# Kernel optimization log

Measured on AMD Instinct MI355X. Metric: run time of the kernel, lower is better.

The kernel has to match this reference:

```python
import jax, jax.numpy as jnp
import numpy as np

# (npoint, radius, nsample) per SA stage, from module defaults
SA_CFG = [(2048, 0.2, 64), (1024, 0.4, 32), (512, 0.6, 16), (256, 1.2, 8)]


def fps(xyz, npoint):
    """Farthest point sampling, CUDA-kernel semantics: start at index 0.
    xyz: [B,N,3] -> idx [B,npoint] int32."""
    B, N, _ = xyz.shape

    def step(carry, _):
        dist, far = carry
        centroid = jnp.take_along_axis(xyz, far[:, None, None], axis=1)  # [B,1,3]
        d = jnp.sum((xyz - centroid) ** 2, axis=-1)                      # [B,N]
        dist = jnp.minimum(dist, d)
        return (dist, jnp.argmax(dist, axis=-1).astype(jnp.int32)), far

    init = (jnp.full((B, N), 1e10, xyz.dtype), jnp.zeros((B,), jnp.int32))
    _, idxs = jax.lax.scan(step, init, None, length=npoint)  # [npoint,B]
    return idxs.T


def gather(pts, idx):
    """pts: [B,N,C], idx: [B,...] int -> [B,...,C]."""
    return jax.vmap(lambda p, i: p[i])(pts, idx)


def ball_query(xyz, new_xyz, radius, nsample):
    """First-nsample-in-ball semantics of pointnet2 ball_query; pads with the
    first found neighbor. xyz:[B,N,3], new_xyz:[B,S,3] -> [B,S,nsample] int."""
    N = xyz.shape[1]
    # squared dists via ||a||^2 + ||b||^2 - 2ab to avoid a [B,S,N,3] temp
    d2 = (jnp.sum(new_xyz ** 2, -1)[:, :, None]
          + jnp.sum(xyz ** 2, -1)[:, None, :]
          - 2.0 * jnp.einsum('bsc,bnc->bsn', new_xyz, xyz))
    cand = jnp.where(d2 < radius * radius, jnp.arange(N)[None, None, :], N)
    idx = jnp.sort(cand, axis=-1)[..., :nsample]
    first = idx[..., :1]  # center itself is always in the ball (d2==0)
    return jnp.where(idx == N, first, idx)


def sa_stage(xyz, feats, npoint, radius, nsample, layers):
    """One PointnetSAModuleVotes: FPS + ball query + normalized relative xyz
    (use_xyz=True, normalize_xyz=True) + shared MLP + max pool over nsample."""
    fidx = fps(xyz, npoint)
    new_xyz = gather(xyz, fidx)                         # [B,S,3]
    nidx = ball_query(xyz, new_xyz, radius, nsample)    # [B,S,K]
    rel = (gather(xyz, nidx) - new_xyz[:, :, None, :]) / radius  # [B,S,K,3]
    x = rel if feats is None else jnp.concatenate([rel, gather(feats, nidx)], -1)
    for w, b in layers:  # shared 1x1-conv MLP (BN folded), ReLU
        x = jax.nn.relu(x @ w + b)
    return new_xyz, jnp.max(x, axis=2)                  # [B,S,C_out]


def setup_inputs() -> dict:
    key = jax.random.key(0)
    ks = jax.random.split(key, 16)
    inp = {"pointcloud": jax.random.normal(ks[0], (4, 16384, 3), jnp.float32)}
    dims = [(3, 64, 64, 128), (131, 128, 128, 256),
            (259, 256, 256, 512), (515, 512, 512, 512)]
    k = 1
    for s, d in enumerate(dims, 1):
        for l in range(3):
            inp[f"w{s}{l}"] = jax.random.normal(
                jax.random.fold_in(ks[k], l), (d[l], d[l + 1]), jnp.float32) * 0.02
            inp[f"b{s}{l}"] = jnp.zeros((d[l + 1],), jnp.float32)
        k += 1
    return inp


def reference(pointcloud,
              w10, b10, w11, b11, w12, b12,
              w20, b20, w21, b21, w22, b22,
              w30, b30, w31, b31, w32, b32,
              w40, b40, w41, b41, w42, b42):
    stage_params = [
        [(w10, b10), (w11, b11), (w12, b12)],
        [(w20, b20), (w21, b21), (w22, b22)],
        [(w30, b30), (w31, b31), (w32, b32)],
        [(w40, b40), (w41, b41), (w42, b42)],
    ]
    xyz = pointcloud[..., :3]
    feats = None  # input_feature_dim == 0
    for (npoint, radius, nsample), layers in zip(SA_CFG, stage_params):
        xyz, feats = sa_stage(xyz, feats, npoint, radius, nsample, layers)
    return xyz, feats  # sa4_xyz [B,256,3], sa4_features [B,256,512]
```

## Files before the change

### kernel.cpp

```cpp
#include <hip/hip_runtime.h>
#include <hip/hip_bf16.h>


#define B_SZ 4

typedef float v2f __attribute__((ext_vector_type(2)));

__device__ __forceinline__ v2f pk_add(v2f a, v2f b) {
  v2f d;
  asm("v_pk_add_f32 %0, %1, %2" : "=v"(d) : "v"(a), "v"(b));
  return d;
}
__device__ __forceinline__ v2f pk_mul(v2f a, v2f b) {
  v2f d;
  asm("v_pk_mul_f32 %0, %1, %2" : "=v"(d) : "v"(a), "v"(b));
  return d;
}

template <int CTRL>
__device__ __forceinline__ unsigned long long dpp_u64(unsigned long long v) {
  int lo = (int)(unsigned)v;
  int hi = (int)(unsigned)(v >> 32);
  int nlo = __builtin_amdgcn_update_dpp(lo, lo, CTRL, 0xF, 0xF, false);
  int nhi = __builtin_amdgcn_update_dpp(hi, hi, CTRL, 0xF, 0xF, false);
  return ((unsigned long long)(unsigned)nhi << 32) | (unsigned)nlo;
}

__device__ __forceinline__ unsigned long long wave_max_u64(unsigned long long P) {
  unsigned long long o;
  o = dpp_u64<0x111>(P); P = o > P ? o : P;
  o = dpp_u64<0x112>(P); P = o > P ? o : P;
  o = dpp_u64<0x114>(P); P = o > P ? o : P;
  o = dpp_u64<0x118>(P); P = o > P ? o : P;
  o = dpp_u64<0x142>(P); P = o > P ? o : P;
  o = dpp_u64<0x143>(P); P = o > P ? o : P;
  return P;
}

template <int N, int NPOINT, int T, bool XYZ_IN_LDS>
__global__ __launch_bounds__(T) void fps_kernel(const float* __restrict__ xyz,
                                                int* __restrict__ fidx) {
#pragma clang fp contract(off)
  constexpr int PT = N / T;
  static_assert(PT % 2 == 0, "PT even");
  constexpr int NP2 = PT / 2;
  constexpr int NW = T / 64;
  constexpr int NCH = (NP2 >= 4) ? 4 : NP2;
  constexpr int CW = NP2 / NCH;
  constexpr int LN = XYZ_IN_LDS ? N : 1;
  const int b = blockIdx.x;
  const int t = threadIdx.x;
  const int lane = t & 63;
  const int wv = t >> 6;
  const float* base = xyz + (size_t)b * N * 3;

  v2f px[NP2], py[NP2], pz[NP2], dv[NP2];
  __shared__ __align__(16) unsigned long long s_pack[2][NW];
  __shared__ float s_x[LN], s_y[LN], s_z[LN];

#pragma unroll
  for (int j = 0; j < NP2; ++j) {
    int i0 = t + (2 * j) * T;
    int i1 = t + (2 * j + 1) * T;
    px[j][0] = base[i0 * 3 + 0];
    py[j][0] = base[i0 * 3 + 1];
    pz[j][0] = base[i0 * 3 + 2];
    px[j][1] = base[i1 * 3 + 0];
    py[j][1] = base[i1 * 3 + 1];
    pz[j][1] = base[i1 * 3 + 2];
    dv[j][0] = 1e10f;
    dv[j][1] = 1e10f;
    if constexpr (XYZ_IN_LDS) {
      s_x[i0] = px[j][0];
      s_y[i0] = py[j][0];
      s_z[i0] = pz[j][0];
      s_x[i1] = px[j][1];
      s_y[i1] = py[j][1];
      s_z[i1] = pz[j][1];
    }
  }
  __syncthreads();

  int far = 0;
  int p = 0;
  for (int it = 0; it < NPOINT; ++it) {
    if (t == 0) fidx[b * NPOINT + it] = far;
    float cx, cy, cz;
    if constexpr (XYZ_IN_LDS) {
      cx = s_x[far];
      cy = s_y[far];
      cz = s_z[far];
    } else {
      cx = base[far * 3 + 0];
      cy = base[far * 3 + 1];
      cz = base[far * 3 + 2];
    }
    const float nx = -cx, ny = -cy, nz = -cz;
    const v2f c2x = {nx, nx}, c2y = {ny, ny}, c2z = {nz, nz};

    float best[NCH];
    int bk[NCH];
#pragma unroll
    for (int q = 0; q < NCH; ++q) {
      best[q] = -1.0f;
      bk[q] = 0;
    }

#pragma unroll
    for (int j = 0; j < NP2; ++j) {
      v2f dx = pk_add(px[j], c2x);
      v2f dy = pk_add(py[j], c2y);
      v2f dz = pk_add(pz[j], c2z);
      v2f xx = pk_mul(dx, dx);
      v2f yy = pk_mul(dy, dy);
      v2f zz = pk_mul(dz, dz);
      v2f s = pk_add(xx, yy);
      v2f d = pk_add(s, zz);
      v2f nd;
      nd[0] = fminf(dv[j][0], d[0]);
      nd[1] = fminf(dv[j][1], d[1]);
      dv[j] = nd;
      const int q = j / CW;
      if (nd[0] > best[q]) {
        best[q] = nd[0];
        bk[q] = 2 * j;
      }
      if (nd[1] > best[q]) {
        best[q] = nd[1];
        bk[q] = 2 * j + 1;
      }
    }
    float bb = best[0];
    int kk = bk[0];
#pragma unroll
    for (int q = 1; q < NCH; ++q) {
      if (best[q] > bb) {
        bb = best[q];
        kk = bk[q];
      }
    }
    int idx = t + kk * T;
    unsigned long long P =
        ((unsigned long long)__float_as_uint(bb) << 32) |
        (unsigned int)(N - idx);
    P = wave_max_u64(P);
    if (lane == 63) s_pack[p][wv] = P;
    __syncthreads();
    unsigned long long bbp = s_pack[p][0];
#pragma unroll
    for (int w = 1; w < NW; ++w) {
      unsigned long long v = s_pack[p][w];
      bbp = v > bbp ? v : bbp;
    }
    far = N - (int)(unsigned int)(bbp & 0xffffffffull);
    p ^= 1;
  }
}

__global__ void gather_xyz_kernel(const float* __restrict__ xyz,
                                  const int* __restrict__ fidx,
                                  float* __restrict__ out, int N, int S) {
  int s = blockIdx.x * blockDim.x + threadIdx.x;
  int b = blockIdx.y;
  if (s < S) {
    int i = fidx[b * S + s];
    out[((size_t)(b * S + s)) * 3 + 0] = xyz[((size_t)(b * N + i)) * 3 + 0];
    out[((size_t)(b * S + s)) * 3 + 1] = xyz[((size_t)(b * N + i)) * 3 + 1];
    out[((size_t)(b * S + s)) * 3 + 2] = xyz[((size_t)(b * N + i)) * 3 + 2];
  }
}

template <int N, int NS>
__global__ __launch_bounds__(256) void ball_query_kernel(
    const float* __restrict__ xyz, const float* __restrict__ new_xyz,
    int* __restrict__ nidx, int S, float r2) {
#pragma clang fp contract(off)
  const int wv = threadIdx.x >> 6;
  const int lane = threadIdx.x & 63;
  const int b = blockIdx.y;
  const int s = blockIdx.x * 4 + wv;
  __shared__ int s_idx[4][NS];
  const float* base = xyz + (size_t)b * N * 3;

  float cx = new_xyz[((size_t)(b * S + s)) * 3 + 0];
  float cy = new_xyz[((size_t)(b * S + s)) * 3 + 1];
  float cz = new_xyz[((size_t)(b * S + s)) * 3 + 2];
  float sc = (cx * cx + cy * cy) + cz * cz;

  int found = 0;
  for (int i0 = 0; i0 < N && found < NS; i0 += 64) {
    int i = i0 + lane;
    float x = base[i * 3 + 0];
    float y = base[i * 3 + 1];
    float z = base[i * 3 + 2];
    float sx = (x * x + y * y) + z * z;
    float dt = (cx * x + cy * y) + cz * z;
    float d2 = (sc + sx) - 2.0f * dt;
    bool inb = d2 < r2;
    unsigned long long m = __ballot(inb);
    if (inb) {
      int pos = found + __popcll(m & ((1ull << lane) - 1));
      if (pos < NS) s_idx[wv][pos] = i;
    }
    found += __popcll(m);
  }
  __syncthreads();
  int fcnt = found < NS ? found : NS;
  int first = s_idx[wv][0];
  int* outp = nidx + ((size_t)(b * S + s)) * NS;
  for (int j = lane; j < NS; j += 64) outp[j] = (j < fcnt) ? s_idx[wv][j] : first;
}

template <int R, int RG, int CG, int CMAXP, int CIN, int COUT>
__device__ __forceinline__ void mlp_layer(float* act, const float* __restrict__ w,
                                          const float* __restrict__ bias, int tid) {
  constexpr int RPT = R / RG;
  constexpr int CPT = COUT / CG;
  static_assert(RG * CG == 256, "thread grid");
  const int rg = tid / CG;
  const int cg = tid % CG;

  float acc[RPT][CPT];
#pragma unroll
  for (int rr = 0; rr < RPT; ++rr)
#pragma unroll
    for (int cc = 0; cc < CPT; ++cc) acc[rr][cc] = 0.f;

  constexpr int K4 = (CIN / 4) * 4;
  for (int k = 0; k < K4; k += 4) {
    float4 a[RPT];
#pragma unroll
    for (int rr = 0; rr < RPT; ++rr)
      a[rr] = *(const float4*)(&act[(rg * RPT + rr) * CMAXP + k]);
    float wvv[4][CPT];
#pragma unroll
    for (int kk = 0; kk < 4; ++kk)
#pragma unroll
      for (int cc = 0; cc < CPT; ++cc)
        wvv[kk][cc] = w[(size_t)(k + kk) * COUT + cg + cc * CG];
#pragma unroll
    for (int rr = 0; rr < RPT; ++rr) {
      float4 av = a[rr];
#pragma unroll
      for (int cc = 0; cc < CPT; ++cc) {
        acc[rr][cc] += av.x * wvv[0][cc];
        acc[rr][cc] += av.y * wvv[1][cc];
        acc[rr][cc] += av.z * wvv[2][cc];
        acc[rr][cc] += av.w * wvv[3][cc];
      }
    }
  }
#pragma unroll 1
  for (int k = K4; k < CIN; ++k) {
    float wvv[CPT];
#pragma unroll
    for (int cc = 0; cc < CPT; ++cc) wvv[cc] = w[(size_t)k * COUT + cg + cc * CG];
#pragma unroll
    for (int rr = 0; rr < RPT; ++rr) {
      float av = act[(rg * RPT + rr) * CMAXP + k];
#pragma unroll
      for (int cc = 0; cc < CPT; ++cc) acc[rr][cc] += av * wvv[cc];
    }
  }
  __syncthreads();
#pragma unroll
  for (int rr = 0; rr < RPT; ++rr)
#pragma unroll
    for (int cc = 0; cc < CPT; ++cc) {
      int co = cg + cc * CG;
      float v = acc[rr][cc] + bias[co];
      act[(rg * RPT + rr) * CMAXP + co] = fmaxf(v, 0.f);
    }
  __syncthreads();
}

template <int NS, int G, int CPREV, int CO0, int CO1, int CO2, int RG, int CG, int CMAXP>
__global__ __launch_bounds__(256) void group_mlp_kernel(
    const float* __restrict__ xyz, const float* __restrict__ new_xyz,
    const float* __restrict__ feats, const int* __restrict__ nidx,
    const float* __restrict__ w0, const float* __restrict__ b0,
    const float* __restrict__ w1, const float* __restrict__ b1,
    const float* __restrict__ w2, const float* __restrict__ b2,
    float* __restrict__ out, int N, int S, float radius) {
  constexpr int R = NS * G;
  constexpr int CIN = 3 + CPREV;
  __shared__ __align__(16) float act[R * CMAXP];
  const int tid = threadIdx.x;
  const int b = blockIdx.y;
  const int s0 = blockIdx.x * G;

  for (int i = tid; i < R * CIN; i += 256) {
    int row = i / CIN;
    int ch = i - row * CIN;
    int g = row / NS;
    int j = row - g * NS;
    int sidx = s0 + g;
    int n = nidx[((size_t)(b * S + sidx)) * NS + j];
    float v;
    if constexpr (CPREV == 0) {
      v = (xyz[((size_t)(b * N + n)) * 3 + ch] -
           new_xyz[((size_t)(b * S + sidx)) * 3 + ch]) /
          radius;
    } else {
      if (ch < 3) {
        v = (xyz[((size_t)(b * N + n)) * 3 + ch] -
             new_xyz[((size_t)(b * S + sidx)) * 3 + ch]) /
            radius;
      } else {
        v = feats[((size_t)(b * N + n)) * CPREV + (ch - 3)];
      }
    }
    act[row * CMAXP + ch] = v;
  }
  __syncthreads();

  mlp_layer<R, RG, CG, CMAXP, CIN, CO0>(act, w0, b0, tid);
  mlp_layer<R, RG, CG, CMAXP, CO0, CO1>(act, w1, b1, tid);
  mlp_layer<R, RG, CG, CMAXP, CO1, CO2>(act, w2, b2, tid);

  for (int i = tid; i < G * CO2; i += 256) {
    int g = i / CO2;
    int co = i - g * CO2;
    float m = act[(g * NS) * CMAXP + co];
    for (int j = 1; j < NS; ++j) m = fmaxf(m, act[(g * NS + j) * CMAXP + co]);
    out[((size_t)(b * S + s0 + g)) * CO2 + co] = m;
  }
}

extern "C" void kernel_launch(void* const* d_in, const int* in_sizes, int n_in,
                              void* d_out, int out_size, void* d_ws, size_t ws_size,
                              hipStream_t stream) {
  (void)in_sizes; (void)n_in; (void)out_size; (void)ws_size;
  const float* pc = (const float*)d_in[0];
  const float* W[4][3];
  const float* Bb[4][3];
  for (int s = 0; s < 4; ++s)
    for (int l = 0; l < 3; ++l) {
      W[s][l] = (const float*)d_in[1 + s * 6 + l * 2];
      Bb[s][l] = (const float*)d_in[2 + s * 6 + l * 2];
    }

  char* wsp = (char*)d_ws;
  int* fidx = (int*)wsp;
  int* nidx = (int*)(wsp + (32 << 10));
  float* xyzA = (float*)(wsp + (32 << 10) + (2 << 20));
  float* xyzB = xyzA + B_SZ * 2048 * 3;
  float* featA = xyzB + B_SZ * 2048 * 3;
  float* featB = featA + B_SZ * 2048 * 128;
  float* oxyz = (float*)d_out;
  float* ofeat = oxyz + B_SZ * 256 * 3;

  hipLaunchKernelGGL((fps_kernel<16384, 2048, 512, false>), dim3(B_SZ), dim3(512), 0, stream,
                     pc, fidx);
  hipLaunchKernelGGL(gather_xyz_kernel, dim3(32, B_SZ), dim3(64), 0, stream,
                     pc, fidx, xyzA, 16384, 2048);
  hipLaunchKernelGGL((ball_query_kernel<16384, 64>), dim3(512, B_SZ), dim3(256), 0, stream,
                     pc, xyzA, nidx, 2048, (float)(0.2 * 0.2));
  hipLaunchKernelGGL((group_mlp_kernel<64, 1, 0, 64, 64, 128, 8, 32, 128>),
                     dim3(2048, B_SZ), dim3(256), 0, stream,
                     pc, xyzA, (const float*)nullptr, nidx,
                     W[0][0], Bb[0][0], W[0][1], Bb[0][1], W[0][2], Bb[0][2],
                     featA, 16384, 2048, 0.2f);

  hipLaunchKernelGGL((fps_kernel<2048, 1024, 512, true>), dim3(B_SZ), dim3(512), 0, stream,
                     xyzA, fidx);
  hipLaunchKernelGGL(gather_xyz_kernel, dim3(16, B_SZ), dim3(64), 0, stream,
                     xyzA, fidx, xyzB, 2048, 1024);
  hipLaunchKernelGGL((ball_query_kernel<2048, 32>), dim3(256, B_SZ), dim3(256), 0, stream,
                     xyzA, xyzB, nidx, 1024, (float)(0.4 * 0.4));
  hipLaunchKernelGGL((group_mlp_kernel<32, 1, 128, 128, 128, 256, 4, 64, 256>),
                     dim3(1024, B_SZ), dim3(256), 0, stream,
                     xyzA, xyzB, featA, nidx,
                     W[1][0], Bb[1][0], W[1][1], Bb[1][1], W[1][2], Bb[1][2],
                     featB, 2048, 1024, 0.4f);

  hipLaunchKernelGGL((fps_kernel<1024, 512, 256, true>), dim3(B_SZ), dim3(256), 0, stream,
                     xyzB, fidx);
  hipLaunchKernelGGL(gather_xyz_kernel, dim3(8, B_SZ), dim3(64), 0, stream,
                     xyzB, fidx, xyzA, 1024, 512);
  hipLaunchKernelGGL((ball_query_kernel<1024, 16>), dim3(128, B_SZ), dim3(256), 0, stream,
                     xyzB, xyzA, nidx, 512, (float)(0.6 * 0.6));
  hipLaunchKernelGGL((group_mlp_kernel<16, 1, 256, 256, 256, 512, 2, 128, 512>),
                     dim3(512, B_SZ), dim3(256), 0, stream,
                     xyzB, xyzA, featB, nidx,
                     W[2][0], Bb[2][0], W[2][1], Bb[2][1], W[2][2], Bb[2][2],
                     featA, 1024, 512, 0.6f);

  hipLaunchKernelGGL((fps_kernel<512, 256, 256, true>), dim3(B_SZ), dim3(256), 0, stream,
                     xyzA, fidx);
  hipLaunchKernelGGL(gather_xyz_kernel, dim3(4, B_SZ), dim3(64), 0, stream,
                     xyzA, fidx, oxyz, 512, 256);
  hipLaunchKernelGGL((ball_query_kernel<512, 8>), dim3(64, B_SZ), dim3(256), 0, stream,
                     xyzA, oxyz, nidx, 256, (float)(1.2 * 1.2));
  hipLaunchKernelGGL((group_mlp_kernel<8, 2, 512, 512, 512, 512, 2, 128, 516>),
                     dim3(128, B_SZ), dim3(256), 0, stream,
                     xyzA, oxyz, featA, nidx,
                     W[3][0], Bb[3][0], W[3][1], Bb[3][1], W[3][2], Bb[3][2],
                     ofeat, 512, 256, 1.2f);
}
```

Before: 5.275 ms.

## Spatially bucket points for stage-1 FPS and skip distant clusters per iteration

Adds a new stage-1 FPS kernel that sorts the points into an 8x8x8 spatial grid, using a histogram, prefix scan and scatter through workspace, so each thread owns a spatially compact cluster of 32 points. Each iteration a thread computes a lower bound from its cluster's bounding sphere to the new centroid and skips the distance update when that bound cannot lower its current maximum. The argmax reduction now carries the winning coordinates as a payload, so the next centroid is read without a global memory load. The changes aim to cut per-iteration ALU and memory work in the serial FPS loop, at the cost of setup passes, workspace aliasing into featB, and branch divergence within waves.

```diff
diff --git a/kernel.cpp b/kernel.cpp
--- a/kernel.cpp
+++ b/kernel.cpp
@@ -5,6 +5,7 @@
 #define B_SZ 4
 
 typedef float v2f __attribute__((ext_vector_type(2)));
+typedef unsigned long long u64;
 
 __device__ __forceinline__ v2f pk_add(v2f a, v2f b) {
   v2f d;
@@ -18,16 +19,36 @@
 }
 
 template <int CTRL>
-__device__ __forceinline__ unsigned long long dpp_u64(unsigned long long v) {
+__device__ __forceinline__ u64 dpp_u64(u64 v) {
   int lo = (int)(unsigned)v;
   int hi = (int)(unsigned)(v >> 32);
   int nlo = __builtin_amdgcn_update_dpp(lo, lo, CTRL, 0xF, 0xF, false);
   int nhi = __builtin_amdgcn_update_dpp(hi, hi, CTRL, 0xF, 0xF, false);
-  return ((unsigned long long)(unsigned)nhi << 32) | (unsigned)nlo;
-}
-
-__device__ __forceinline__ unsigned long long wave_max_u64(unsigned long long P) {
-  unsigned long long o;
+  return ((u64)(unsigned)nhi << 32) | (unsigned)nlo;
+}
+template <int CTRL>
+__device__ __forceinline__ float dpp_f(float v) {
+  int x = __float_as_int(v);
+  return __int_as_float(__builtin_amdgcn_update_dpp(x, x, CTRL, 0xF, 0xF, false));
+}
+
+template <int CTRL>
+__device__ __forceinline__ void red_step(u64& K, float& X, float& Y, float& Z) {
+  u64 oK = dpp_u64<CTRL>(K);
+  float oX = dpp_f<CTRL>(X), oY = dpp_f<CTRL>(Y), oZ = dpp_f<CTRL>(Z);
+  if (oK > K) { K = oK; X = oX; Y = oY; Z = oZ; }
+}
+__device__ __forceinline__ void wave_max_payload(u64& K, float& X, float& Y, float& Z) {
+  red_step<0x111>(K, X, Y, Z);
+  red_step<0x112>(K, X, Y, Z);
+  red_step<0x114>(K, X, Y, Z);
+  red_step<0x118>(K, X, Y, Z);
+  red_step<0x142>(K, X, Y, Z);
+  red_step<0x143>(K, X, Y, Z);
+}
+
+__device__ __forceinline__ u64 wave_max_u64(u64 P) {
+  u64 o;
   o = dpp_u64<0x111>(P); P = o > P ? o : P;
   o = dpp_u64<0x112>(P); P = o > P ? o : P;
   o = dpp_u64<0x114>(P); P = o > P ? o : P;
@@ -35,6 +56,194 @@
   o = dpp_u64<0x142>(P); P = o > P ? o : P;
   o = dpp_u64<0x143>(P); P = o > P ? o : P;
   return P;
+}
+
+template <int N, int NPOINT, int T>
+__global__ __launch_bounds__(T) void fps_bucket_kernel(
+    const float* __restrict__ xyz, int* __restrict__ fidx,
+    float* __restrict__ gsx, float* __restrict__ gsy,
+    float* __restrict__ gsz, int* __restrict__ gsi) {
+#pragma clang fp contract(off)
+  constexpr int PT = N / T;
+  constexpr int NP2 = PT / 2;
+  constexpr int NW = T / 64;
+  constexpr int NB = 512;
+  static_assert(T == NB, "one bin per thread");
+  const int b = blockIdx.x;
+  const int t = threadIdx.x;
+  const int lane = t & 63;
+  const int wv = t >> 6;
+  const float* base = xyz + (size_t)b * N * 3;
+  float* bsx = gsx + (size_t)b * N;
+  float* bsy = gsy + (size_t)b * N;
+  float* bsz = gsz + (size_t)b * N;
+  int* bsi = gsi + (size_t)b * N;
+
+  __shared__ int s_hist[NB];
+  __shared__ int s_scan[NB];
+  __shared__ float s_red[6][NW];
+  __shared__ u64 s_key[2][NW];
+  __shared__ float s_px[2][NW], s_py[2][NW], s_pz[2][NW];
+
+  float mnx = 1e30f, mny = 1e30f, mnz = 1e30f;
+  float mxx = -1e30f, mxy = -1e30f, mxz = -1e30f;
+  for (int k = 0; k < PT; ++k) {
+    int i = t + k * T;
+    float x = base[i * 3 + 0], y = base[i * 3 + 1], z = base[i * 3 + 2];
+    mnx = fminf(mnx, x); mny = fminf(mny, y); mnz = fminf(mnz, z);
+    mxx = fmaxf(mxx, x); mxy = fmaxf(mxy, y); mxz = fmaxf(mxz, z);
+  }
+#pragma unroll
+  for (int off = 1; off < 64; off <<= 1) {
+    mnx = fminf(mnx, __shfl_xor(mnx, off));
+    mny = fminf(mny, __shfl_xor(mny, off));
+    mnz = fminf(mnz, __shfl_xor(mnz, off));
+    mxx = fmaxf(mxx, __shfl_xor(mxx, off));
+    mxy = fmaxf(mxy, __shfl_xor(mxy, off));
+    mxz = fmaxf(mxz, __shfl_xor(mxz, off));
+  }
+  if (lane == 0) {
+    s_red[0][wv] = mnx; s_red[1][wv] = mny; s_red[2][wv] = mnz;
+    s_red[3][wv] = mxx; s_red[4][wv] = mxy; s_red[5][wv] = mxz;
+  }
+  s_hist[t] = 0;
+  __syncthreads();
+  mnx = s_red[0][0]; mny = s_red[1][0]; mnz = s_red[2][0];
+  mxx = s_red[3][0]; mxy = s_red[4][0]; mxz = s_red[5][0];
+#pragma unroll
+  for (int w = 1; w < NW; ++w) {
+    mnx = fminf(mnx, s_red[0][w]); mny = fminf(mny, s_red[1][w]);
+    mnz = fminf(mnz, s_red[2][w]);
+    mxx = fmaxf(mxx, s_red[3][w]); mxy = fmaxf(mxy, s_red[4][w]);
+    mxz = fmaxf(mxz, s_red[5][w]);
+  }
+  const float fx = 8.0f / (mxx - mnx + 1e-5f);
+  const float fy = 8.0f / (mxy - mny + 1e-5f);
+  const float fz = 8.0f / (mxz - mnz + 1e-5f);
+
+  for (int k = 0; k < PT; ++k) {
+    int i = t + k * T;
+    float x = base[i * 3 + 0], y = base[i * 3 + 1], z = base[i * 3 + 2];
+    int cx = min(7, max(0, (int)((x - mnx) * fx)));
+    int cy = min(7, max(0, (int)((y - mny) * fy)));
+    int cz = min(7, max(0, (int)((z - mnz) * fz)));
+    atomicAdd(&s_hist[(cx * 8 + cy) * 8 + cz], 1);
+  }
+  __syncthreads();
+
+  s_scan[t] = s_hist[t];
+  __syncthreads();
+  for (int off = 1; off < NB; off <<= 1) {
+    int v = (t >= off) ? s_scan[t - off] : 0;
+    __syncthreads();
+    s_scan[t] += v;
+    __syncthreads();
+  }
+  s_hist[t] = s_scan[t] - s_hist[t];
+  __syncthreads();
+
+  for (int k = 0; k < PT; ++k) {
+    int i = t + k * T;
+    float x = base[i * 3 + 0], y = base[i * 3 + 1], z = base[i * 3 + 2];
+    int cx = min(7, max(0, (int)((x - mnx) * fx)));
+    int cy = min(7, max(0, (int)((y - mny) * fy)));
+    int cz = min(7, max(0, (int)((z - mnz) * fz)));
+    int pos = atomicAdd(&s_hist[(cx * 8 + cy) * 8 + cz], 1);
+    bsx[pos] = x; bsy[pos] = y; bsz[pos] = z; bsi[pos] = i;
+  }
+  __threadfence();
+  __syncthreads();
+
+  v2f px[NP2], py[NP2], pz[NP2], dv[NP2];
+  unsigned lo[PT];
+#pragma unroll
+  for (int k = 0; k < PT; ++k) {
+    int pos = t * PT + k;
+    float x = bsx[pos], y = bsy[pos], z = bsz[pos];
+    px[k / 2][k & 1] = x; py[k / 2][k & 1] = y; pz[k / 2][k & 1] = z;
+    dv[k / 2][k & 1] = 1e10f;
+    lo[k] = (unsigned)(N - bsi[pos]);
+  }
+  float cmnx = 1e30f, cmny = 1e30f, cmnz = 1e30f;
+  float cmxx = -1e30f, cmxy = -1e30f, cmxz = -1e30f;
+#pragma unroll
+  for (int k = 0; k < PT; ++k) {
+    float x = px[k / 2][k & 1], y = py[k / 2][k & 1], z = pz[k / 2][k & 1];
+    cmnx = fminf(cmnx, x); cmny = fminf(cmny, y); cmnz = fminf(cmnz, z);
+    cmxx = fmaxf(cmxx, x); cmxy = fmaxf(cmxy, y); cmxz = fmaxf(cmxz, z);
+  }
+  const float ccx = 0.5f * (cmnx + cmxx);
+  const float ccy = 0.5f * (cmny + cmxy);
+  const float ccz = 0.5f * (cmnz + cmxz);
+  float r2m = 0.f;
+#pragma unroll
+  for (int k = 0; k < PT; ++k) {
+    float dx = px[k / 2][k & 1] - ccx, dy = py[k / 2][k & 1] - ccy,
+          dz = pz[k / 2][k & 1] - ccz;
+    r2m = fmaxf(r2m, dx * dx + dy * dy + dz * dz);
+  }
+  const float crad = sqrtf(r2m) * 1.0001f + 1e-7f;
+
+  u64 ck = 0;
+  float cbx = 0.f, cby = 0.f, cbz = 0.f, cmax = 1e10f;
+
+  float cenx = base[0], ceny = base[1], cenz = base[2];
+  int far = 0;
+  int p = 0;
+
+  for (int it = 0; it < NPOINT; ++it) {
+    if (t == 0) fidx[b * NPOINT + it] = far;
+
+    float ddx = ccx - cenx, ddy = ccy - ceny, ddz = ccz - cenz;
+    float dc = sqrtf(ddx * ddx + ddy * ddy + ddz * ddz);
+    float lb = dc - crad;
+    bool skip = (lb > 0.f) && (lb * lb * 0.9999f >= cmax * 1.0001f);
+    if (!skip) {
+      const float nx = -cenx, ny = -ceny, nz = -cenz;
+      const v2f c2x = {nx, nx}, c2y = {ny, ny}, c2z = {nz, nz};
+      u64 bkA = 0, bkB = 0;
+      float axA = 0, ayA = 0, azA = 0, axB = 0, ayB = 0, azB = 0;
+#pragma unroll
+      for (int j = 0; j < NP2; ++j) {
+        v2f dx = pk_add(px[j], c2x);
+        v2f dy = pk_add(py[j], c2y);
+        v2f dz = pk_add(pz[j], c2z);
+        v2f xx = pk_mul(dx, dx);
+        v2f yy = pk_mul(dy, dy);
+        v2f zz = pk_mul(dz, dz);
+        v2f s = pk_add(xx, yy);
+        v2f d = pk_add(s, zz);
+        float nd0 = fminf(dv[j][0], d[0]);
+        float nd1 = fminf(dv[j][1], d[1]);
+        dv[j][0] = nd0; dv[j][1] = nd1;
+        u64 p0 = ((u64)__float_as_uint(nd0) << 32) | lo[2 * j];
+        if (p0 > bkA) { bkA = p0; axA = px[j][0]; ayA = py[j][0]; azA = pz[j][0]; }
+        u64 p1 = ((u64)__float_as_uint(nd1) << 32) | lo[2 * j + 1];
+        if (p1 > bkB) { bkB = p1; axB = px[j][1]; ayB = py[j][1]; azB = pz[j][1]; }
+      }
+      if (bkB > bkA) { bkA = bkB; axA = axB; ayA = ayB; azA = azB; }
+      ck = bkA; cbx = axA; cby = ayA; cbz = azA;
+      cmax = __uint_as_float((unsigned)(bkA >> 32));
+    }
+
+    u64 K = ck;
+    float X = cbx, Y = cby, Z = cbz;
+    wave_max_payload(K, X, Y, Z);
+    if (lane == 63) {
+      s_key[p][wv] = K; s_px[p][wv] = X; s_py[p][wv] = Y; s_pz[p][wv] = Z;
+    }
+    __syncthreads();
+    u64 bb = s_key[p][0];
+    int m = 0;
+#pragma unroll
+    for (int w = 1; w < NW; ++w) {
+      u64 v = s_key[p][w];
+      if (v > bb) { bb = v; m = w; }
+    }
+    far = N - (int)(unsigned)(bb & 0xffffffffull);
+    cenx = s_px[p][m]; ceny = s_py[p][m]; cenz = s_pz[p][m];
+    p ^= 1;
+  }
 }
 
 template <int N, int NPOINT, int T, bool XYZ_IN_LDS>
@@ -55,28 +264,21 @@
   const float* base = xyz + (size_t)b * N * 3;
 
   v2f px[NP2], py[NP2], pz[NP2], dv[NP2];
-  __shared__ __align__(16) unsigned long long s_pack[2][NW];
+  __shared__ __align__(16) u64 s_pack[2][NW];
   __shared__ float s_x[LN], s_y[LN], s_z[LN];
 
 #pragma unroll
   for (int j = 0; j < NP2; ++j) {
     int i0 = t + (2 * j) * T;
     int i1 = t + (2 * j + 1) * T;
-    px[j][0] = base[i0 * 3 + 0];
-    py[j][0] = base[i0 * 3 + 1];
+    px[j][0] = base[i0 * 3 + 0]; py[j][0] = base[i0 * 3 + 1];
     pz[j][0] = base[i0 * 3 + 2];
-    px[j][1] = base[i1 * 3 + 0];
-    py[j][1] = base[i1 * 3 + 1];
+    px[j][1] = base[i1 * 3 + 0]; py[j][1] = base[i1 * 3 + 1];
     pz[j][1] = base[i1 * 3 + 2];
-    dv[j][0] = 1e10f;
-    dv[j][1] = 1e10f;
+    dv[j][0] = 1e10f; dv[j][1] = 1e10f;
     if constexpr (XYZ_IN_LDS) {
-      s_x[i0] = px[j][0];
-      s_y[i0] = py[j][0];
-      s_z[i0] = pz[j][0];
-      s_x[i1] = px[j][1];
-      s_y[i1] = py[j][1];
-      s_z[i1] = pz[j][1];
+      s_x[i0] = px[j][0]; s_y[i0] = py[j][0]; s_z[i0] = pz[j][0];
+      s_x[i1] = px[j][1]; s_y[i1] = py[j][1]; s_z[i1] = pz[j][1];
     }
   }
   __syncthreads();
@@ -87,13 +289,9 @@
     if (t == 0) fidx[b * NPOINT + it] = far;
     float cx, cy, cz;
     if constexpr (XYZ_IN_LDS) {
-      cx = s_x[far];
-      cy = s_y[far];
-      cz = s_z[far];
+      cx = s_x[far]; cy = s_y[far]; cz = s_z[far];
     } else {
-      cx = base[far * 3 + 0];
-      cy = base[far * 3 + 1];
-      cz = base[far * 3 + 2];
+      cx = base[far * 3 + 0]; cy = base[far * 3 + 1]; cz = base[far * 3 + 2];
     }
     const float nx = -cx, ny = -cy, nz = -cz;
     const v2f c2x = {nx, nx}, c2y = {ny, ny}, c2z = {nz, nz};
@@ -101,10 +299,7 @@
     float best[NCH];
     int bk[NCH];
 #pragma unroll
-    for (int q = 0; q < NCH; ++q) {
-      best[q] = -1.0f;
-      bk[q] = 0;
-    }
+    for (int q = 0; q < NCH; ++q) { best[q] = -1.0f; bk[q] = 0; }
 
 #pragma unroll
     for (int j = 0; j < NP2; ++j) {
@@ -121,38 +316,27 @@
       nd[1] = fminf(dv[j][1], d[1]);
       dv[j] = nd;
       const int q = j / CW;
-      if (nd[0] > best[q]) {
-        best[q] = nd[0];
-        bk[q] = 2 * j;
-      }
-      if (nd[1] > best[q]) {
-        best[q] = nd[1];
-        bk[q] = 2 * j + 1;
-      }
+      if (nd[0] > best[q]) { best[q] = nd[0]; bk[q] = 2 * j; }
+      if (nd[1] > best[q]) { best[q] = nd[1]; bk[q] = 2 * j + 1; }
     }
     float bb = best[0];
     int kk = bk[0];
 #pragma unroll
     for (int q = 1; q < NCH; ++q) {
-      if (best[q] > bb) {
-        bb = best[q];
-        kk = bk[q];
-      }
+      if (best[q] > bb) { bb = best[q]; kk = bk[q]; }
     }
     int idx = t + kk * T;
-    unsigned long long P =
-        ((unsigned long long)__float_as_uint(bb) << 32) |
-        (unsigned int)(N - idx);
+    u64 P = ((u64)__float_as_uint(bb) << 32) | (unsigned)(N - idx);
     P = wave_max_u64(P);
     if (lane == 63) s_pack[p][wv] = P;
     __syncthreads();
-    unsigned long long bbp = s_pack[p][0];
+    u64 bbp = s_pack[p][0];
 #pragma unroll
     for (int w = 1; w < NW; ++w) {
-      unsigned long long v = s_pack[p][w];
+      u64 v = s_pack[p][w];
       bbp = v > bbp ? v : bbp;
     }
-    far = N - (int)(unsigned int)(bbp & 0xffffffffull);
+    far = N - (int)(unsigned)(bbp & 0xffffffffull);
     p ^= 1;
   }
 }
@@ -347,11 +531,15 @@
   float* xyzB = xyzA + B_SZ * 2048 * 3;
   float* featA = xyzB + B_SZ * 2048 * 3;
   float* featB = featA + B_SZ * 2048 * 128;
+  float* gsx = featB;
+  float* gsy = gsx + B_SZ * 16384;
+  float* gsz = gsy + B_SZ * 16384;
+  int* gsi = (int*)(gsz + B_SZ * 16384);
   float* oxyz = (float*)d_out;
   float* ofeat = oxyz + B_SZ * 256 * 3;
 
-  hipLaunchKernelGGL((fps_kernel<16384, 2048, 512, false>), dim3(B_SZ), dim3(512), 0, stream,
-                     pc, fidx);
+  hipLaunchKernelGGL((fps_bucket_kernel<16384, 2048, 512>), dim3(B_SZ), dim3(512), 0, stream,
+                     pc, fidx, gsx, gsy, gsz, gsi);
   hipLaunchKernelGGL(gather_xyz_kernel, dim3(32, B_SZ), dim3(64), 0, stream,
                      pc, fidx, xyzA, 16384, 2048);
   hipLaunchKernelGGL((ball_query_kernel<16384, 64>), dim3(512, B_SZ), dim3(256), 0, stream,
```

Result: slower. 7.528 ms (+42.7%).
